# Kernel tuning notes

Hardware: AMD Instinct MI355X
Metric: run time of the kernel (lower is better)

The kernel has to match this reference:

```python
import jax, jax.numpy as jnp
import numpy as np

# dims
B, S, D, H, DH, M, L, V, BS, NR = 4, 2048, 512, 8, 64, 2048, 6, 32000, 64, 3
NB = S // BS  # 32 blocks


def _block_plan(nb, seed):
    """BigBird block connectivity: 2 global + 3 window + NR random blocks per query block.
    Returns idx [nb, K] int32 and validity mask [nb, K] bool (dedup + edge handling)."""
    rng = np.random.RandomState(seed)
    K = 5 + NR
    idx = np.zeros((nb, K), np.int32)
    msk = np.zeros((nb, K), bool)
    for i in range(nb):
        fixed = {0, nb - 1} | {j for j in (i - 1, i, i + 1) if 0 <= j < nb}
        rest = [j for j in range(nb) if j not in fixed]
        rnd = rng.choice(rest, size=min(NR, len(rest)), replace=False) if rest else []
        sel = sorted(fixed | set(int(r) for r in rnd))
        idx[i, :len(sel)] = sel
        msk[i, :len(sel)] = True
    return jnp.asarray(idx), jnp.asarray(msk)


def _posemb():
    pos = np.arange(S, dtype=np.float32)[:, None]
    div = np.exp(np.arange(0, D, 2, dtype=np.float32) * (-np.log(10000.0) / D))
    pe = np.zeros((S, D), np.float32)
    pe[:, 0::2] = np.sin(pos * div)
    pe[:, 1::2] = np.cos(pos * div)
    return jnp.asarray(pe)


def _ln(x, scale, bias):
    m = jnp.mean(x, axis=-1, keepdims=True)
    v = jnp.mean(jnp.square(x - m), axis=-1, keepdims=True)
    return (x - m) * jax.lax.rsqrt(v + 1e-6) * scale + bias


def _bigbird_attn(x, key_mask, wq, wk, wv, wo, idx, bmask):
    # x: [B,S,D]; idx/bmask: [NB,K]
    q = jnp.einsum('bsd,dhe->bshe', x, wq).reshape(B, NB, BS, H, DH)
    k = jnp.einsum('bsd,dhe->bshe', x, wk).reshape(B, NB, BS, H, DH)
    v = jnp.einsum('bsd,dhe->bshe', x, wv).reshape(B, NB, BS, H, DH)
    kg = k[:, idx]  # [B,NB,K,BS,H,DH] gathered key blocks
    vg = v[:, idx]
    scores = jnp.einsum('bnqhe,bnkche->bhnqkc', q, kg) / jnp.sqrt(jnp.float32(DH))
    kmb = key_mask.reshape(B, NB, BS)[:, idx]          # [B,NB,K,BS]
    m = kmb & bmask[None, :, :, None]                   # [B,NB,K,BS]
    scores = jnp.where(m[:, None, :, None, :, :], scores, jnp.float32(-1e9))
    Kc = idx.shape[1]
    attn = jax.nn.softmax(scores.reshape(B, H, NB, BS, Kc * BS), axis=-1)
    attn = attn.reshape(B, H, NB, BS, Kc, BS)
    out = jnp.einsum('bhnqkc,bnkche->bnqhe', attn, vg).reshape(B, S, H, DH)
    return jnp.einsum('bshe,hed->bsd', out, wo)


def setup_inputs() -> dict:
    key = jax.random.key(0)
    ks = jax.random.split(key, 12)
    n = jax.random.normal
    inp = {
        'tokens': jax.random.randint(ks[0], (B, S), 0, V, dtype=jnp.int32),
        'embed': n(ks[1], (V, D), dtype=jnp.float32),
        'ln1_s': jnp.ones((L, D), jnp.float32), 'ln1_b': jnp.zeros((L, D), jnp.float32),
        'wq': n(ks[2], (L, D, H, DH), dtype=jnp.float32) * 0.02,
        'wk': n(ks[3], (L, D, H, DH), dtype=jnp.float32) * 0.02,
        'wv': n(ks[4], (L, D, H, DH), dtype=jnp.float32) * 0.02,
        'wo': n(ks[5], (L, H, DH, D), dtype=jnp.float32) * 0.02,
        'ln2_s': jnp.ones((L, D), jnp.float32), 'ln2_b': jnp.zeros((L, D), jnp.float32),
        'w1': n(ks[6], (L, D, M), dtype=jnp.float32) * 0.02, 'b1': jnp.zeros((L, M), jnp.float32),
        'w2': n(ks[7], (L, M, D), dtype=jnp.float32) * 0.02, 'b2': jnp.zeros((L, D), jnp.float32),
        'lnf_s': jnp.ones((D,), jnp.float32), 'lnf_b': jnp.zeros((D,), jnp.float32),
    }
    return inp


def reference(tokens, embed, ln1_s, ln1_b, wq, wk, wv, wo, ln2_s, ln2_b, w1, b1, w2, b2, lnf_s, lnf_b):
    key_mask = tokens > 0                      # src padding mask
    x = embed[tokens] + _posemb()[None]        # [B,S,D]
    plans = [_block_plan(NB, l) for l in range(L)]  # connectivity_seed = layer index
    for l in range(L):
        idx, bm = plans[l]
        h = _ln(x, ln1_s[l], ln1_b[l])
        x = x + _bigbird_attn(h, key_mask, wq[l], wk[l], wv[l], wo[l], idx, bm)
        y = _ln(x, ln2_s[l], ln2_b[l])
        y = jax.nn.gelu(jnp.einsum('bsd,dm->bsm', y, w1[l]) + b1[l])
        y = jnp.einsum('bsm,md->bsd', y, w2[l]) + b2[l]
        x = x + y
    return _ln(x, lnf_s, lnf_b)
```

## Files before the change

### kernel.cpp

```cpp
#include <hip/hip_runtime.h>

using u32 = unsigned int;
using u16 = unsigned short;

#define B_   4
#define S_   2048
#define D_   512
#define H_   8
#define DH_  64
#define FF_  2048
#define L_   6
#define NB_  32
#define KC_  8

typedef __attribute__((ext_vector_type(8))) __bf16 bf16x8;
typedef __attribute__((ext_vector_type(4))) float  f32x4;

struct Plan { unsigned char idx[NB_][KC_]; unsigned char cnt[NB_]; };

__device__ __forceinline__ u16 f2b(float f) {
  union { float f; u32 u; } x; x.f = f;
  u32 u = x.u;
  u32 r = (u + 0x7fffu + ((u >> 16) & 1u)) >> 16;
  return (u16)r;
}

__device__ __forceinline__ float gelu_f(float x) {
  float y2 = 1.5957691216f * x + 0.0713548163f * x * x * x;
  return x / (1.0f + __expf(-y2));
}

typedef const __attribute__((address_space(1))) u32* gas_t;
typedef __attribute__((address_space(3))) u32* las_t;
__device__ __forceinline__ void glds16(const u16* g, u16* l) {
  __builtin_amdgcn_global_load_lds((gas_t)g, (las_t)l, 16, 0, 0);
}

__global__ __launch_bounds__(256)
void transpose_conv(const float* __restrict__ in, u16* __restrict__ out, int R, int C,
                    size_t lstride, int rowoff) {
  __shared__ float tile[32][33];
  const int l = blockIdx.z;
  const float* src = in + (size_t)l * R * C;
  u16* dst = out + (size_t)l * lstride;
  const int c0 = blockIdx.x * 32, r0 = blockIdx.y * 32;
  const int tx = threadIdx.x, ty = threadIdx.y;
#pragma unroll
  for (int i = 0; i < 4; i++)
    tile[ty + i * 8][tx] = src[(size_t)(r0 + ty + i * 8) * C + c0 + tx];
  __syncthreads();
#pragma unroll
  for (int i = 0; i < 4; i++)
    dst[(size_t)(rowoff + c0 + ty + i * 8) * R + r0 + tx] = f2b(tile[tx][ty + i * 8]);
}

__global__ __launch_bounds__(128)
void embed_kernel(const int* __restrict__ tokens, const float* __restrict__ emb,
                  float* __restrict__ x) {
  const int row = blockIdx.x;
  const int s = row & (S_ - 1);
  const int t = threadIdx.x;
  const int tok = tokens[row];
  float4 v = ((const float4*)(emb + (size_t)tok * D_))[t];
  float va[4] = {v.x, v.y, v.z, v.w};
  const float cc = -2.0f * logf(10000.0f) / (float)D_;
  const float pos = (float)s;
#pragma unroll
  for (int j = 0; j < 4; j++) {
    int d = t * 4 + j;
    int i = d >> 1;
    float dv = expf(cc * (float)i);
    float ang = pos * dv;
    va[j] += (d & 1) ? cosf(ang) : sinf(ang);
  }
  ((float4*)x)[(size_t)row * (D_ / 4) + t] = make_float4(va[0], va[1], va[2], va[3]);
}

template <bool BF16OUT>
__global__ __launch_bounds__(128)
void ln_kernel(const float* __restrict__ x, const float* __restrict__ sc,
               const float* __restrict__ bi, void* __restrict__ outp) {
  const int row = blockIdx.x;
  const int t = threadIdx.x;
  float4 v = ((const float4*)(x + (size_t)row * D_))[t];
  float va[4] = {v.x, v.y, v.z, v.w};
  float s = va[0] + va[1] + va[2] + va[3];
  float sq = va[0] * va[0] + va[1] * va[1] + va[2] * va[2] + va[3] * va[3];
#pragma unroll
  for (int d = 1; d < 64; d <<= 1) {
    s  += __shfl_xor(s, d);
    sq += __shfl_xor(sq, d);
  }
  __shared__ float red[4];
  const int wv = t >> 6, lane = t & 63;
  if (lane == 0) { red[wv * 2] = s; red[wv * 2 + 1] = sq; }
  __syncthreads();
  const float ts  = red[0] + red[2];
  const float tsq = red[1] + red[3];
  const float mean = ts * (1.0f / (float)D_);
  const float inv  = rsqrtf(tsq * (1.0f / (float)D_) - mean * mean + 1e-6f);
  const int d0 = t * 4;
  float o[4];
#pragma unroll
  for (int j = 0; j < 4; j++)
    o[j] = (va[j] - mean) * inv * sc[d0 + j] + bi[d0 + j];
  if (BF16OUT) {
    ushort4 u;
    u.x = f2b(o[0]); u.y = f2b(o[1]); u.z = f2b(o[2]); u.w = f2b(o[3]);
    ((ushort4*)outp)[(size_t)row * (D_ / 4) + t] = u;
  } else {
    ((float4*)outp)[(size_t)row * (D_ / 4) + t] = make_float4(o[0], o[1], o[2], o[3]);
  }
}

template <int MODE, int BN, bool VSPLIT>
__global__ __launch_bounds__(256)
void gemm_bt(const u16* __restrict__ A, const u16* __restrict__ BT,
             int Kk, int ostride,
             float* __restrict__ outf, u16* __restrict__ outb,
             const float* __restrict__ bias, const float* __restrict__ resid,
             u16* __restrict__ vtout) {
  constexpr int MI  = (BN == 128) ? 4 : 2;
  constexpr int BCH = BN / 64;
  __shared__ u16 As[2][128 * 32];
  __shared__ u16 Bs[2][BN * 32];
  const int tid = threadIdx.x;
  const int wave = tid >> 6, lane = tid & 63;
  const int row0 = blockIdx.x * 128, col0 = blockIdx.y * BN;
  const int wr = (BN == 128) ? (wave >> 1) : wave;
  const int wc = (BN == 128) ? (wave & 1) : 0;
  const int l15 = lane & 15, l4 = lane >> 4;

  const u16* asrc[2];
  int adst[2];
#pragma unroll
  for (int i = 0; i < 2; i++) {
    int c0 = wave * 128 + i * 64;
    int cl = c0 + lane;
    int r = cl >> 2, s = cl & 3;
    asrc[i] = A + (size_t)(row0 + r) * Kk + ((s ^ ((r >> 1) & 3)) << 3);
    adst[i] = c0 * 8;
  }
  const u16* bsrc[BCH];
  int bdst[BCH];
#pragma unroll
  for (int i = 0; i < BCH; i++) {
    int c0 = wave * (BCH * 64) + i * 64;
    int cl = c0 + lane;
    int r = cl >> 2, s = cl & 3;
    bsrc[i] = BT + (size_t)(col0 + r) * Kk + ((s ^ ((r >> 1) & 3)) << 3);
    bdst[i] = c0 * 8;
  }

  const int swz = (l4 ^ ((l15 >> 1) & 3)) << 3;
  int aoff[MI], boff[4];
#pragma unroll
  for (int m = 0; m < MI; m++) aoff[m] = (wr * (MI * 16) + m * 16 + l15) * 32 + swz;
#pragma unroll
  for (int n = 0; n < 4; n++)  boff[n] = (wc * 64 + n * 16 + l15) * 32 + swz;

  f32x4 acc[MI][4] = {};
  const int nk = Kk >> 5;

#pragma unroll
  for (int i = 0; i < 2; i++) glds16(asrc[i], &As[0][adst[i]]);
#pragma unroll
  for (int i = 0; i < BCH; i++) glds16(bsrc[i], &Bs[0][bdst[i]]);

  for (int t = 0; t < nk; ++t) {
    const int cur = t & 1;
    __syncthreads();
    if (t + 1 < nk) {
      const int ko = (t + 1) << 5;
#pragma unroll
      for (int i = 0; i < 2; i++) glds16(asrc[i] + ko, &As[cur ^ 1][adst[i]]);
#pragma unroll
      for (int i = 0; i < BCH; i++) glds16(bsrc[i] + ko, &Bs[cur ^ 1][bdst[i]]);
    }
    bf16x8 af[MI], bfr[4];
#pragma unroll
    for (int m = 0; m < MI; m++) af[m] = *(const bf16x8*)&As[cur][aoff[m]];
#pragma unroll
    for (int n = 0; n < 4; n++)  bfr[n] = *(const bf16x8*)&Bs[cur][boff[n]];
#pragma unroll
    for (int m = 0; m < MI; m++)
#pragma unroll
      for (int n = 0; n < 4; n++)
        acc[m][n] = __builtin_amdgcn_mfma_f32_16x16x32_bf16(af[m], bfr[n], acc[m][n], 0, 0, 0);
  }

#pragma unroll
  for (int m = 0; m < MI; m++) {
#pragma unroll
    for (int n = 0; n < 4; n++) {
      const int c = col0 + wc * 64 + n * 16 + l15;
      const int rb = row0 + wr * (MI * 16) + m * 16 + l4 * 4;
      if (VSPLIT && c >= 1024) {
        u16 pk[4];
#pragma unroll
        for (int j = 0; j < 4; j++) pk[j] = f2b(acc[m][n][j]);
        *(uint2*)(vtout + (size_t)(c - 1024) * (B_ * S_) + rb) = *(const uint2*)pk;
      } else {
#pragma unroll
        for (int j = 0; j < 4; j++) {
          const size_t o = (size_t)(rb + j) * ostride + c;
          float v = acc[m][n][j];
          if (MODE == 0) {
            outb[o] = f2b(v);
          } else if (MODE == 1) {
            outf[o] = v + resid[o];
          } else if (MODE == 2) {
            outb[o] = f2b(gelu_f(v + bias[c]));
          } else {
            outf[o] = v + bias[c] + resid[o];
          }
        }
      }
    }
  }
}

__global__ __launch_bounds__(256)
void attn_mfma(const u16* __restrict__ qkv, const u16* __restrict__ vTg,
               const int* __restrict__ tokens, u16* __restrict__ outb, Plan plan) {
  __shared__ u16 qs[64 * 64];
  __shared__ u16 ks[2][64 * 64];
  __shared__ u16 vt[2][64 * 64];
  __shared__ u16 ps[64 * 64];
  __shared__ unsigned char km[KC_ * 64];

  const int blk = blockIdx.x;
  const int h0 = blk & 7;
  const int n  = (blk >> 3) & 31;
  const int b  = blk >> 8;
  const int t  = threadIdx.x;
  const int wave = t >> 6, lane = t & 63;
  const int l15 = lane & 15, l4 = lane >> 4;
  const int ncnt = plan.cnt[n];
  const int qrow0 = b * S_ + n * 64;

  auto stage = [&](int bi, int c) {
    const int krow0 = b * S_ + c * 64;
#pragma unroll
    for (int i = 0; i < 2; i++) {
      int c0 = i * 256 + wave * 64;
      int cl = c0 + lane;
      int r = cl >> 3, s = cl & 7;
      int sw = (s ^ (r & 7)) << 3;
      glds16(qkv + (size_t)(krow0 + r) * 1024 + 512 + h0 * 64 + sw, &ks[bi][c0 * 8]);
      glds16(vTg + (size_t)(h0 * 64 + r) * (B_ * S_) + krow0 + sw, &vt[bi][c0 * 8]);
    }
  };

#pragma unroll
  for (int i = 0; i < 2; i++) {
    int c0 = i * 256 + wave * 64;
    int cl = c0 + lane;
    int r = cl >> 3, s = cl & 7;
    glds16(qkv + (size_t)(qrow0 + r) * 1024 + h0 * 64 + ((s ^ (r & 7)) << 3), qs + c0 * 8);
  }
#pragma unroll
  for (int i = 0; i < 2; i++) {
    int e = t + i * 256;
    int kc = e >> 6, col = e & 63;
    int c = plan.idx[n][kc];
    km[e] = (kc < ncnt) && (tokens[b * S_ + c * 64 + col] > 0);
  }
  stage(0, plan.idx[n][0]);

  f32x4 oacc[4] = {};
  float mrow[4], lrow[4];
#pragma unroll
  for (int j = 0; j < 4; j++) { mrow[j] = -3e38f; lrow[j] = 0.0f; }

  for (int kc = 0; kc < ncnt; kc++) {
    const int cur = kc & 1;
    __syncthreads();
    if (kc + 1 < ncnt) stage(cur ^ 1, plan.idx[n][kc + 1]);

    bf16x8 qaf[2];
#pragma unroll
    for (int ks_ = 0; ks_ < 2; ks_++) {
      int r = wave * 16 + l15;
      qaf[ks_] = *(const bf16x8*)(qs + r * 64 + ((ks_ * 32 + l4 * 8) ^ ((r & 7) << 3)));
    }

    f32x4 sacc[4] = {};
#pragma unroll
    for (int nn = 0; nn < 4; nn++) {
      int r = nn * 16 + l15;
#pragma unroll
      for (int ks_ = 0; ks_ < 2; ks_++) {
        bf16x8 kf = *(const bf16x8*)(&ks[cur][r * 64 + ((ks_ * 32 + l4 * 8) ^ ((r & 7) << 3))]);
        sacc[nn] = __builtin_amdgcn_mfma_f32_16x16x32_bf16(qaf[ks_], kf, sacc[nn], 0, 0, 0);
      }
    }

    bool vld[4];
#pragma unroll
    for (int nn = 0; nn < 4; nn++) vld[nn] = km[kc * 64 + nn * 16 + l15] != 0;

    float p[4][4], rmax[4], alpha[4];
#pragma unroll
    for (int j = 0; j < 4; j++) {
      float mj = -3e38f;
#pragma unroll
      for (int nn = 0; nn < 4; nn++) {
        float sv = sacc[nn][j] * 0.125f;
        p[nn][j] = sv;
        if (vld[nn]) mj = fmaxf(mj, sv);
      }
      rmax[j] = mj;
    }
#pragma unroll
    for (int d = 1; d < 16; d <<= 1) {
#pragma unroll
      for (int j = 0; j < 4; j++) rmax[j] = fmaxf(rmax[j], __shfl_xor(rmax[j], d));
    }
#pragma unroll
    for (int j = 0; j < 4; j++) {
      float mn = fmaxf(mrow[j], rmax[j]);
      alpha[j] = __expf(mrow[j] - mn);
      mrow[j] = mn;
      float psum = 0.0f;
#pragma unroll
      for (int nn = 0; nn < 4; nn++) {
        float pv = vld[nn] ? __expf(p[nn][j] - mn) : 0.0f;
        p[nn][j] = pv;
        psum += pv;
      }
      lrow[j] = lrow[j] * alpha[j] + psum;
    }
#pragma unroll
    for (int n2 = 0; n2 < 4; n2++)
#pragma unroll
      for (int j = 0; j < 4; j++) oacc[n2][j] *= alpha[j];

#pragma unroll
    for (int nn = 0; nn < 4; nn++)
#pragma unroll
      for (int j = 0; j < 4; j++) {
        int q = wave * 16 + l4 * 4 + j;
        ps[q * 64 + ((nn * 16 + l15) ^ ((q & 7) << 3))] = f2b(p[nn][j]);
      }

#pragma unroll
    for (int ks_ = 0; ks_ < 2; ks_++) {
      int r = wave * 16 + l15;
      bf16x8 paf = *(const bf16x8*)(ps + r * 64 + ((ks_ * 32 + l4 * 8) ^ ((r & 7) << 3)));
#pragma unroll
      for (int n2 = 0; n2 < 4; n2++) {
        int rv = n2 * 16 + l15;
        bf16x8 vf = *(const bf16x8*)(&vt[cur][rv * 64 + ((ks_ * 32 + l4 * 8) ^ ((rv & 7) << 3))]);
        oacc[n2] = __builtin_amdgcn_mfma_f32_16x16x32_bf16(paf, vf, oacc[n2], 0, 0, 0);
      }
    }
  }

#pragma unroll
  for (int d = 1; d < 16; d <<= 1) {
#pragma unroll
    for (int j = 0; j < 4; j++) lrow[j] += __shfl_xor(lrow[j], d);
  }
#pragma unroll
  for (int j = 0; j < 4; j++) {
    const float inv = lrow[j] > 0.0f ? 1.0f / lrow[j] : 0.0f;
    const int q = n * 64 + wave * 16 + l4 * 4 + j;
#pragma unroll
    for (int n2 = 0; n2 < 4; n2++) {
      outb[(size_t)(b * S_ + q) * D_ + h0 * 64 + n2 * 16 + l15] = f2b(oacc[n2][j] * inv);
    }
  }
}

namespace {
struct HostMT {
  u32 mt[624]; int mti;
  void seed(u32 s) {
    mt[0] = s;
    for (int i = 1; i < 624; i++)
      mt[i] = 1812433253u * (mt[i - 1] ^ (mt[i - 1] >> 30)) + (u32)i;
    mti = 624;
  }
  u32 next() {
    if (mti >= 624) {
      for (int k = 0; k < 624; k++) {
        u32 y = (mt[k] & 0x80000000u) | (mt[(k + 1) % 624] & 0x7fffffffu);
        mt[k] = mt[(k + 397) % 624] ^ (y >> 1) ^ ((y & 1u) ? 0x9908b0dfu : 0u);
      }
      mti = 0;
    }
    u32 y = mt[mti++];
    y ^= y >> 11;
    y ^= (y << 7)  & 0x9d2c5680u;
    y ^= (y << 15) & 0xefc60000u;
    y ^= y >> 18;
    return y;
  }
  u32 interval(u32 mx) {
    if (mx == 0u) return 0u;
    u32 mask = mx;
    mask |= mask >> 1; mask |= mask >> 2; mask |= mask >> 4;
    mask |= mask >> 8; mask |= mask >> 16;
    u32 v;
    while ((v = (next() & mask)) > mx) {}
    return v;
  }
};

void build_plan(int l, Plan* out) {
  HostMT rng;
  rng.seed((u32)l);
  for (int i = 0; i < NB_; i++) {
    bool fixedv[NB_] = {};
    fixedv[0] = true; fixedv[NB_ - 1] = true;
    for (int j = i - 1; j <= i + 1; j++)
      if (j >= 0 && j < NB_) fixedv[j] = true;
    int rest[NB_]; int nr = 0;
    for (int j = 0; j < NB_; j++) if (!fixedv[j]) rest[nr++] = j;
    int perm[NB_];
    for (int tt = 0; tt < nr; tt++) perm[tt] = tt;
    for (int tt = nr - 1; tt >= 1; tt--) {
      int j = (int)rng.interval((u32)tt);
      int tmp = perm[tt]; perm[tt] = perm[j]; perm[j] = tmp;
    }
    bool sel[NB_];
    for (int j = 0; j < NB_; j++) sel[j] = fixedv[j];
    for (int c = 0; c < 3; c++) sel[rest[perm[c]]] = true;
    int cnt = 0;
    for (int j = 0; j < NB_; j++)
      if (sel[j]) out->idx[i][cnt++] = (unsigned char)j;
    out->cnt[i] = (unsigned char)cnt;
    for (int c2 = cnt; c2 < KC_; c2++) out->idx[i][c2] = 0;
  }
}
}

extern "C" void kernel_launch(void* const* d_in, const int* in_sizes, int n_in,
                              void* d_out, int out_size, void* d_ws, size_t ws_size,
                              hipStream_t stream) {
  (void)in_sizes; (void)n_in; (void)out_size; (void)ws_size;

  const int*   tokens = (const int*)d_in[0];
  const float* embed  = (const float*)d_in[1];
  const float* ln1_s  = (const float*)d_in[2];
  const float* ln1_b  = (const float*)d_in[3];
  const float* wq     = (const float*)d_in[4];
  const float* wk     = (const float*)d_in[5];
  const float* wv     = (const float*)d_in[6];
  const float* wo     = (const float*)d_in[7];
  const float* ln2_s  = (const float*)d_in[8];
  const float* ln2_b  = (const float*)d_in[9];
  const float* w1     = (const float*)d_in[10];
  const float* b1     = (const float*)d_in[11];
  const float* w2     = (const float*)d_in[12];
  const float* b2     = (const float*)d_in[13];
  const float* lnf_s  = (const float*)d_in[14];
  const float* lnf_b  = (const float*)d_in[15];

  char* wp = (char*)d_ws;
  auto take = [&](size_t bytes) {
    void* p = (void*)wp;
    wp += (bytes + 255) & ~(size_t)255;
    return p;
  };

  const int Mrows = B_ * S_;
  u16* wqkvT = (u16*)take((size_t)L_ * 1536 * D_ * 2);
  u16* woT   = (u16*)take((size_t)L_ * D_ * D_ * 2);
  u16* w1T   = (u16*)take((size_t)L_ * FF_ * D_ * 2);
  u16* w2T   = (u16*)take((size_t)L_ * D_ * FF_ * 2);
  float* x   = (float*)take((size_t)Mrows * D_ * 4);
  u16* h     = (u16*)take((size_t)Mrows * D_ * 2);
  u16* big   = (u16*)take((size_t)Mrows * FF_ * 2);
  u16* qkv   = big;
  u16* vT    = big + (size_t)Mrows * 1024;
  u16* g     = big;

  Plan plans[L_];
  for (int l = 0; l < L_; l++) build_plan(l, &plans[l]);

  const size_t qkvL = (size_t)1536 * D_;

  transpose_conv<<<dim3(D_ / 32, D_ / 32, L_), dim3(32, 8), 0, stream>>>(wq, wqkvT, D_, D_, qkvL, 0);
  transpose_conv<<<dim3(D_ / 32, D_ / 32, L_), dim3(32, 8), 0, stream>>>(wk, wqkvT, D_, D_, qkvL, 512);
  transpose_conv<<<dim3(D_ / 32, D_ / 32, L_), dim3(32, 8), 0, stream>>>(wv, wqkvT, D_, D_, qkvL, 1024);
  transpose_conv<<<dim3(D_ / 32, D_ / 32, L_), dim3(32, 8), 0, stream>>>(wo, woT, D_, D_, (size_t)D_ * D_, 0);
  transpose_conv<<<dim3(FF_ / 32, D_ / 32, L_), dim3(32, 8), 0, stream>>>(w1, w1T, D_, FF_, (size_t)FF_ * D_, 0);
  transpose_conv<<<dim3(D_ / 32, FF_ / 32, L_), dim3(32, 8), 0, stream>>>(w2, w2T, FF_, D_, (size_t)D_ * FF_, 0);
  embed_kernel<<<Mrows, 128, 0, stream>>>(tokens, embed, x);

  for (int l = 0; l < L_; l++) {
    ln_kernel<true><<<Mrows, 128, 0, stream>>>(x, ln1_s + l * D_, ln1_b + l * D_, h);
    gemm_bt<0, 128, true><<<dim3(Mrows / 128, 12), 256, 0, stream>>>(
        h, wqkvT + (size_t)l * qkvL, D_, 1024, nullptr, qkv, nullptr, nullptr, vT);
    attn_mfma<<<B_ * NB_ * H_, 256, 0, stream>>>(qkv, vT, tokens, h, plans[l]);
    gemm_bt<1, 64, false><<<dim3(Mrows / 128, 8), 256, 0, stream>>>(
        h, woT + (size_t)l * D_ * D_, D_, D_, x, nullptr, nullptr, x, nullptr);
    ln_kernel<true><<<Mrows, 128, 0, stream>>>(x, ln2_s + l * D_, ln2_b + l * D_, h);
    gemm_bt<2, 128, false><<<dim3(Mrows / 128, 16), 256, 0, stream>>>(
        h, w1T + (size_t)l * FF_ * D_, D_, FF_, nullptr, g, b1 + l * FF_, nullptr, nullptr);
    gemm_bt<3, 64, false><<<dim3(Mrows / 128, 8), 256, 0, stream>>>(
        g, w2T + (size_t)l * D_ * FF_, FF_, D_, x, nullptr, b2 + l * D_, x, nullptr);
  }
  ln_kernel<false><<<Mrows, 128, 0, stream>>>(x, lnf_s, lnf_b, d_out);
}
```

Before: 930.1 us.

## Fold softmax scale into Q projection and streamline attention inner loop

Folds the 1/sqrt(dh)*log2(e) factor into Q when the QKV GEMM writes it, so attention can use exp2 directly. Q fragments now load straight from global memory into registers rather than through LDS, and key-mask tokens are prefetched into registers with each K/V stage, which removes the km table and the qs buffer. The online-softmax rescale is skipped when no row maximum changes, launch bounds now request 4 blocks, and f2b uses the native bf16 conversion. Since attention is one part among six layers of GEMMs, the effect on end-to-end time is likely small.

```diff
diff --git a/kernel.cpp b/kernel.cpp
--- a/kernel.cpp
+++ b/kernel.cpp
@@ -18,11 +18,12 @@
 
 struct Plan { unsigned char idx[NB_][KC_]; unsigned char cnt[NB_]; };
 
+#define QSCALE 0.18033688011112042f
+
 __device__ __forceinline__ u16 f2b(float f) {
-  union { float f; u32 u; } x; x.f = f;
-  u32 u = x.u;
-  u32 r = (u + 0x7fffu + ((u >> 16) & 1u)) >> 16;
-  return (u16)r;
+  union { __bf16 b; u16 u; } x;
+  x.b = (__bf16)f;
+  return x.u;
 }
 
 __device__ __forceinline__ float gelu_f(float x) {
@@ -206,6 +207,7 @@
           const size_t o = (size_t)(rb + j) * ostride + c;
           float v = acc[m][n][j];
           if (MODE == 0) {
+            if (VSPLIT && c < 512) v *= QSCALE;
             outb[o] = f2b(v);
           } else if (MODE == 1) {
             outf[o] = v + resid[o];
@@ -220,14 +222,12 @@
   }
 }
 
-__global__ __launch_bounds__(256)
+__global__ __launch_bounds__(256, 4)
 void attn_mfma(const u16* __restrict__ qkv, const u16* __restrict__ vTg,
                const int* __restrict__ tokens, u16* __restrict__ outb, Plan plan) {
-  __shared__ u16 qs[64 * 64];
   __shared__ u16 ks[2][64 * 64];
   __shared__ u16 vt[2][64 * 64];
   __shared__ u16 ps[64 * 64];
-  __shared__ unsigned char km[KC_ * 64];
 
   const int blk = blockIdx.x;
   const int h0 = blk & 7;
@@ -239,7 +239,7 @@
   const int ncnt = plan.cnt[n];
   const int qrow0 = b * S_ + n * 64;
 
-  auto stage = [&](int bi, int c) {
+  auto stage = [&](int bi, int c, int* tkd) {
     const int krow0 = b * S_ + c * 64;
 #pragma unroll
     for (int i = 0; i < 2; i++) {
@@ -250,23 +250,18 @@
       glds16(qkv + (size_t)(krow0 + r) * 1024 + 512 + h0 * 64 + sw, &ks[bi][c0 * 8]);
       glds16(vTg + (size_t)(h0 * 64 + r) * (B_ * S_) + krow0 + sw, &vt[bi][c0 * 8]);
     }
+#pragma unroll
+    for (int nn = 0; nn < 4; nn++) tkd[nn] = tokens[krow0 + nn * 16 + l15];
   };
 
-#pragma unroll
-  for (int i = 0; i < 2; i++) {
-    int c0 = i * 256 + wave * 64;
-    int cl = c0 + lane;
-    int r = cl >> 3, s = cl & 7;
-    glds16(qkv + (size_t)(qrow0 + r) * 1024 + h0 * 64 + ((s ^ (r & 7)) << 3), qs + c0 * 8);
-  }
-#pragma unroll
-  for (int i = 0; i < 2; i++) {
-    int e = t + i * 256;
-    int kc = e >> 6, col = e & 63;
-    int c = plan.idx[n][kc];
-    km[e] = (kc < ncnt) && (tokens[b * S_ + c * 64 + col] > 0);
-  }
-  stage(0, plan.idx[n][0]);
+  bf16x8 qaf[2];
+#pragma unroll
+  for (int ks_ = 0; ks_ < 2; ks_++)
+    qaf[ks_] = *(const bf16x8*)(qkv + (size_t)(qrow0 + wave * 16 + l15) * 1024 +
+                                h0 * 64 + ks_ * 32 + l4 * 8);
+
+  int tk[4], tn[4];
+  stage(0, plan.idx[n][0], tk);
 
   f32x4 oacc[4] = {};
   float mrow[4], lrow[4];
@@ -276,14 +271,7 @@
   for (int kc = 0; kc < ncnt; kc++) {
     const int cur = kc & 1;
     __syncthreads();
-    if (kc + 1 < ncnt) stage(cur ^ 1, plan.idx[n][kc + 1]);
-
-    bf16x8 qaf[2];
-#pragma unroll
-    for (int ks_ = 0; ks_ < 2; ks_++) {
-      int r = wave * 16 + l15;
-      qaf[ks_] = *(const bf16x8*)(qs + r * 64 + ((ks_ * 32 + l4 * 8) ^ ((r & 7) << 3)));
-    }
+    if (kc + 1 < ncnt) stage(cur ^ 1, plan.idx[n][kc + 1], tn);
 
     f32x4 sacc[4] = {};
 #pragma unroll
@@ -298,43 +286,48 @@
 
     bool vld[4];
 #pragma unroll
-    for (int nn = 0; nn < 4; nn++) vld[nn] = km[kc * 64 + nn * 16 + l15] != 0;
-
-    float p[4][4], rmax[4], alpha[4];
+    for (int nn = 0; nn < 4; nn++) vld[nn] = tk[nn] > 0;
+
+    float rmax[4];
 #pragma unroll
     for (int j = 0; j < 4; j++) {
       float mj = -3e38f;
 #pragma unroll
+      for (int nn = 0; nn < 4; nn++)
+        if (vld[nn]) mj = fmaxf(mj, sacc[nn][j]);
+      rmax[j] = mj;
+    }
+#pragma unroll
+    for (int d = 1; d < 16; d <<= 1) {
+#pragma unroll
+      for (int j = 0; j < 4; j++) rmax[j] = fmaxf(rmax[j], __shfl_xor(rmax[j], d));
+    }
+    int chg = 0;
+#pragma unroll
+    for (int j = 0; j < 4; j++) chg |= (rmax[j] > mrow[j]);
+    if (__ballot(chg)) {
+#pragma unroll
+      for (int j = 0; j < 4; j++) {
+        float mn = fmaxf(mrow[j], rmax[j]);
+        float alpha = exp2f(mrow[j] - mn);
+        mrow[j] = mn;
+        lrow[j] *= alpha;
+#pragma unroll
+        for (int n2 = 0; n2 < 4; n2++) oacc[n2][j] *= alpha;
+      }
+    }
+    float p[4][4];
+#pragma unroll
+    for (int j = 0; j < 4; j++) {
+      float psum = 0.0f;
+#pragma unroll
       for (int nn = 0; nn < 4; nn++) {
-        float sv = sacc[nn][j] * 0.125f;
-        p[nn][j] = sv;
-        if (vld[nn]) mj = fmaxf(mj, sv);
-      }
-      rmax[j] = mj;
-    }
-#pragma unroll
-    for (int d = 1; d < 16; d <<= 1) {
-#pragma unroll
-      for (int j = 0; j < 4; j++) rmax[j] = fmaxf(rmax[j], __shfl_xor(rmax[j], d));
-    }
-#pragma unroll
-    for (int j = 0; j < 4; j++) {
-      float mn = fmaxf(mrow[j], rmax[j]);
-      alpha[j] = __expf(mrow[j] - mn);
-      mrow[j] = mn;
-      float psum = 0.0f;
-#pragma unroll
-      for (int nn = 0; nn < 4; nn++) {
-        float pv = vld[nn] ? __expf(p[nn][j] - mn) : 0.0f;
+        float pv = vld[nn] ? exp2f(sacc[nn][j] - mrow[j]) : 0.0f;
         p[nn][j] = pv;
         psum += pv;
       }
-      lrow[j] = lrow[j] * alpha[j] + psum;
-    }
-#pragma unroll
-    for (int n2 = 0; n2 < 4; n2++)
-#pragma unroll
-      for (int j = 0; j < 4; j++) oacc[n2][j] *= alpha[j];
+      lrow[j] += psum;
+    }
 
 #pragma unroll
     for (int nn = 0; nn < 4; nn++)
@@ -355,6 +348,8 @@
         oacc[n2] = __builtin_amdgcn_mfma_f32_16x16x32_bf16(paf, vf, oacc[n2], 0, 0, 0);
       }
     }
+#pragma unroll
+    for (int nn = 0; nn < 4; nn++) tk[nn] = tn[nn];
   }
 
 #pragma unroll
```

New measurement: 923.1 us. No clear change (-0.8%).
